# Kernel optimization log

Measured on AMD Instinct MI355X. Metric: run time of the kernel, lower is better.

Reference implementation:

```python
import jax, jax.numpy as jnp
import numpy as np

B, C, K = 8192, 4096, 4096
BK, BN = 1, 16          # block-sparse tile sizes (bk x bn)
KEEP = 0.3


def setup_inputs() -> dict:
    key = jax.random.key(0)
    kx, kw, kb, km = jax.random.split(key, 4)
    stdv = 1.0 / np.sqrt(C * K)  # reset_parameters uses 1/sqrt(C*K)
    x = jax.random.normal(kx, (B, C), dtype=jnp.float32)
    weight = jax.random.uniform(kw, (K, C), dtype=jnp.float32, minval=-stdv, maxval=stdv)
    # block mask on (K/bk, C/bn) grid, expanded to full weight shape
    blk = (jax.random.uniform(km, (K // BK, C // BN)) < KEEP).astype(jnp.float32)
    mask = jnp.repeat(jnp.repeat(blk, BK, axis=0), BN, axis=1)  # [K, C]
    weight = weight * mask
    bias = jax.random.uniform(kb, (K,), dtype=jnp.float32, minval=-stdv, maxval=stdv)
    return {"x": x, "weight": weight, "bias": bias}


def reference(x, weight, bias):
    # SparseLinearRelu forward (sparse-kernel path, attr='relu'):
    # y = relu(x @ W^T + b); zero blocks of W contribute nothing (skipped by kernel).
    return jax.nn.relu(jnp.dot(x, weight.T) + bias)
```

## Files before the change

kernel.cpp:

```cpp
#include <hip/hip_runtime.h>
#include <hip/hip_bf16.h>

typedef __attribute__((ext_vector_type(4))) float f32x4;
typedef __attribute__((ext_vector_type(8))) short bf16x8;
typedef __attribute__((ext_vector_type(4))) short bf16x4v;

#define M_DIM 8192
#define N_DIM 4096
#define K_DIM 4096
#define NX (M_DIM * K_DIM)
#define NW (N_DIM * K_DIM)

#define BM 256
#define BN 256
#define BK 64
#define NKT (K_DIM / BK)
#define THREADS 512

#define GLOAD_LDS16(g, l)                                                        \
  __builtin_amdgcn_global_load_lds(                                              \
      (const __attribute__((address_space(1))) void*)(g),                        \
      (__attribute__((address_space(3))) void*)(l), 16, 0, 0)

__global__ __launch_bounds__(256) void convert_bf16(const float* __restrict__ x,
                                                    const float* __restrict__ w,
                                                    short* __restrict__ ws) {
  const long stride = (long)gridDim.x * blockDim.x;
  const long total8 = ((long)NX + NW) / 8;
  for (long i = blockIdx.x * (long)blockDim.x + threadIdx.x; i < total8; i += stride) {
    const long base = i * 8;
    const float* src = (base < NX) ? (x + base) : (w + (base - NX));
    short* dst = ws + base;
    f32x4 a = *(const f32x4*)src;
    f32x4 b = *(const f32x4*)(src + 4);
    bf16x8 o;
    o[0] = (short)__bfloat16_as_ushort(__float2bfloat16(a[0]));
    o[1] = (short)__bfloat16_as_ushort(__float2bfloat16(a[1]));
    o[2] = (short)__bfloat16_as_ushort(__float2bfloat16(a[2]));
    o[3] = (short)__bfloat16_as_ushort(__float2bfloat16(a[3]));
    o[4] = (short)__bfloat16_as_ushort(__float2bfloat16(b[0]));
    o[5] = (short)__bfloat16_as_ushort(__float2bfloat16(b[1]));
    o[6] = (short)__bfloat16_as_ushort(__float2bfloat16(b[2]));
    o[7] = (short)__bfloat16_as_ushort(__float2bfloat16(b[3]));
    *(bf16x8*)dst = o;
  }
}

__global__ __launch_bounds__(THREADS, 2) void gemm256_bf16(
    const short* __restrict__ Abf,
    const short* __restrict__ Bbf,
    const float* __restrict__ bias,
    float* __restrict__ Y) {
  __shared__ short lds[2 * 32768];
  char* const ldsb = (char*)lds;

  const int tid  = threadIdx.x;
  const int lane = tid & 63;
  const int wave = tid >> 6;
  const int wm   = wave >> 2;
  const int wn   = wave & 3;

  const int lin = blockIdx.x + blockIdx.y * (N_DIM / BN);
  const int xcd = lin & 7;
  const int idx = lin >> 3;
  const int by = (xcd >> 1) * 8 + (idx >> 3);
  const int bx = (xcd & 1) * 8 + (idx & 7);
  const long rowA0 = (long)by * BM;
  const long rowB0 = (long)bx * BN;

  const int sg_col = (((lane & 7) ^ ((lane >> 3) & 7)) << 3);
  const int s_row  = wave * 8 + (lane >> 3);
  const int voff = s_row * K_DIM + sg_col;

  const short* uA = Abf + rowA0 * (long)K_DIM;
  const short* uB = Bbf + rowB0 * (long)K_DIM;

  const int offk0 = (lane & 15) * 128 + ((((lane >> 4)) ^ (lane & 7)) << 4);
  const int offk1 = (lane & 15) * 128 + (((4 + (lane >> 4)) ^ (lane & 7)) << 4);

#define STAGE_HALF(BOFF_, HALF_, TT) do {                                        \
    const short* u_ = ((HALF_) < 2 ? uA : uB) +                                  \
                      (long)(((HALF_) & 1) * 128) * K_DIM + (long)(TT) * BK;     \
    char* l_ = ldsb + (BOFF_) + ((HALF_) < 2 ? 0 : 32768) +                      \
               ((HALF_) & 1) * 16384 + wave * 1024;                              \
    GLOAD_LDS16(u_ + voff, l_);                                                  \
    GLOAD_LDS16(u_ + 64 * K_DIM + voff, l_ + 8192);                              \
  } while (0)

#define PH_READ_A(DST, BOFF_, MADD) do {                                         \
    const char* pa_ = ldsb + (BOFF_) + wm * 16384 + (MADD);                      \
    _Pragma("unroll")                                                            \
    for (int m_ = 0; m_ < 4; ++m_) {                                             \
      DST[m_][0] = *(const bf16x8*)(pa_ + m_ * 2048 + offk0);                    \
      DST[m_][1] = *(const bf16x8*)(pa_ + m_ * 2048 + offk1);                    \
    }                                                                            \
  } while (0)

#define PH_READ_B(DST, BOFF_, NADD) do {                                         \
    const char* pb_ = ldsb + (BOFF_) + 32768 + wn * 8192 + (NADD);               \
    _Pragma("unroll")                                                            \
    for (int n_ = 0; n_ < 2; ++n_) {                                             \
      DST[n_][0] = *(const bf16x8*)(pb_ + n_ * 2048 + offk0);                    \
      DST[n_][1] = *(const bf16x8*)(pb_ + n_ * 2048 + offk1);                    \
    }                                                                            \
  } while (0)

#define MFMA16(AF, BF, MB, NB) do {                                              \
    __builtin_amdgcn_s_setprio(1);                                               \
    _Pragma("unroll")                                                            \
    for (int kk_ = 0; kk_ < 2; ++kk_)                                            \
      _Pragma("unroll")                                                          \
      for (int m_ = 0; m_ < 4; ++m_)                                             \
        _Pragma("unroll")                                                        \
        for (int n_ = 0; n_ < 2; ++n_)                                           \
          acc[(MB) + m_][(NB) + n_] = __builtin_amdgcn_mfma_f32_16x16x32_bf16(   \
              AF[m_][kk_], BF[n_][kk_], acc[(MB) + m_][(NB) + n_], 0, 0, 0);     \
    __builtin_amdgcn_s_setprio(0);                                               \
  } while (0)

#define TILE(BOFF_, T, DO_ST, VM) do {                                           \
                               \
    PH_READ_A(af, BOFF_, 0);                                                     \
    PH_READ_B(bfr01, BOFF_, 0);                                                  \
    MFMA16(af, bfr01, 0, 0);                                                     \
    __builtin_amdgcn_s_barrier();                                                \
                                        \
    PH_READ_B(bfr23, BOFF_, 4096);                                               \
    MFMA16(af, bfr23, 0, 2);                                                     \
    __builtin_amdgcn_s_barrier();                                                \
                          \
    PH_READ_A(af, BOFF_, 8192);                                                  \
    if (DO_ST) { STAGE_HALF(BOFF_, 2, (T) + 2); STAGE_HALF(BOFF_, 3, (T) + 2); } \
    MFMA16(af, bfr01, 4, 0);                                                     \
    __builtin_amdgcn_s_barrier();                                                \
                   \
    if (DO_ST) { STAGE_HALF(BOFF_, 0, (T) + 2); STAGE_HALF(BOFF_, 1, (T) + 2); } \
    MFMA16(af, bfr23, 4, 2);                                                     \
    if ((VM) == 8)      asm volatile("s_waitcnt vmcnt(8)" ::: "memory");         \
    else if ((VM) == 0) asm volatile("s_waitcnt vmcnt(0)" ::: "memory");         \
    if ((VM) >= 0) __builtin_amdgcn_s_barrier();                                 \
  } while (0)

  f32x4 acc[8][4];
#pragma unroll
  for (int i = 0; i < 8; ++i)
#pragma unroll
    for (int j = 0; j < 4; ++j) acc[i][j] = (f32x4)0.0f;

  bf16x8 af[4][2], bfr01[2][2], bfr23[2][2];

  STAGE_HALF(0, 0, 0);
  STAGE_HALF(0, 1, 0);
  STAGE_HALF(0, 2, 0);
  STAGE_HALF(0, 3, 0);
  STAGE_HALF(65536, 2, 1);
  STAGE_HALF(65536, 3, 1);
  STAGE_HALF(65536, 0, 1);
  STAGE_HALF(65536, 1, 1);
  asm volatile("s_waitcnt vmcnt(8)" ::: "memory");
  __builtin_amdgcn_s_barrier();

  for (int tp = 0; tp < NKT / 2 - 1; ++tp) {
    const int t0 = 2 * tp;
    TILE(0,     t0,     1, 8);
    TILE(65536, t0 + 1, 1, 8);
  }
  TILE(0,     NKT - 2, 0, 0);
  TILE(65536, NKT - 1, 0, -1);

#undef TILE
#undef MFMA16
#undef PH_READ_B
#undef PH_READ_A
#undef STAGE_HALF

  {
    char* scr = ldsb + wave * 8192;
    const int c0 = lane & 15;
    const int r0 = (lane >> 4) * 4;
    const int rd_row = lane >> 3;
    const int rd_ch  = (lane & 7) * 16;
#pragma unroll
    for (int jp = 0; jp < 2; ++jp) {
      const long gcb = rowB0 + wn * 64 + jp * 32 + (lane & 7) * 4;
      const f32x4 bv4 = *(const f32x4*)&bias[gcb];
#pragma unroll
      for (int i = 0; i < 8; ++i) {
#pragma unroll
        for (int r = 0; r < 4; ++r) {
          *(float*)(scr + (r0 + r) * 144 + c0 * 4)      = acc[i][2 * jp + 0][r];
          *(float*)(scr + (r0 + r) * 144 + 64 + c0 * 4) = acc[i][2 * jp + 1][r];
        }
        f32x4 v0 = *(const f32x4*)(scr + rd_row * 144 + rd_ch);
        f32x4 v1 = *(const f32x4*)(scr + (8 + rd_row) * 144 + rd_ch);
        v0 += bv4;
        v1 += bv4;
#pragma unroll
        for (int e = 0; e < 4; ++e) {
          v0[e] = fmaxf(v0[e], 0.0f);
          v1[e] = fmaxf(v1[e], 0.0f);
        }
        const long gr = rowA0 + wm * 128 + i * 16;
        *(f32x4*)&Y[(gr + rd_row) * (long)N_DIM + gcb]     = v0;
        *(f32x4*)&Y[(gr + 8 + rd_row) * (long)N_DIM + gcb] = v1;
      }
    }
  }
}

#define FBM 128
#define FBK 32
#define FLDSS 40
__global__ __launch_bounds__(256) void fallback_gemm(
    const float* __restrict__ X, const float* __restrict__ W,
    const float* __restrict__ bias, float* __restrict__ Y) {
  __shared__ short As[FBM * FLDSS];
  __shared__ short Bs[FBM * FLDSS];
  const int tid = threadIdx.x, lane = tid & 63, wave = tid >> 6;
  const int wm = (wave >> 1) * 64, wn = (wave & 1) * 64;
  const long rowA0 = (long)blockIdx.y * FBM, rowB0 = (long)blockIdx.x * FBM;
  const int srow = tid >> 3, scol = (tid & 7) * 4;
  const float* Aptr = X + (rowA0 + srow) * (long)K_DIM + scol;
  const float* Bptr = W + (rowB0 + srow) * (long)K_DIM + scol;
  f32x4 ra[4], rb[4];
#pragma unroll
  for (int i = 0; i < 4; ++i) {
    ra[i] = *(const f32x4*)(Aptr + (long)i * 32 * K_DIM);
    rb[i] = *(const f32x4*)(Bptr + (long)i * 32 * K_DIM);
  }
  f32x4 acc[4][4];
#pragma unroll
  for (int i = 0; i < 4; ++i)
#pragma unroll
    for (int j = 0; j < 4; ++j) acc[i][j] = (f32x4)0.0f;
  for (int kt = 0; kt < K_DIM / FBK; ++kt) {
    __syncthreads();
#pragma unroll
    for (int i = 0; i < 4; ++i) {
      bf16x4v pa, pb;
#pragma unroll
      for (int j = 0; j < 4; ++j) {
        pa[j] = (short)__bfloat16_as_ushort(__float2bfloat16(ra[i][j]));
        pb[j] = (short)__bfloat16_as_ushort(__float2bfloat16(rb[i][j]));
      }
      *(bf16x4v*)&As[(i * 32 + srow) * FLDSS + scol] = pa;
      *(bf16x4v*)&Bs[(i * 32 + srow) * FLDSS + scol] = pb;
    }
    if (kt + 1 < K_DIM / FBK) {
      const float* An = Aptr + (kt + 1) * FBK;
      const float* Bn = Bptr + (kt + 1) * FBK;
#pragma unroll
      for (int i = 0; i < 4; ++i) {
        ra[i] = *(const f32x4*)(An + (long)i * 32 * K_DIM);
        rb[i] = *(const f32x4*)(Bn + (long)i * 32 * K_DIM);
      }
    }
    __syncthreads();
    bf16x8 af[4], bfr[4];
#pragma unroll
    for (int i = 0; i < 4; ++i) {
      af[i]  = *(const bf16x8*)&As[(wm + i * 16 + (lane & 15)) * FLDSS + (lane >> 4) * 8];
      bfr[i] = *(const bf16x8*)&Bs[(wn + i * 16 + (lane & 15)) * FLDSS + (lane >> 4) * 8];
    }
#pragma unroll
    for (int i = 0; i < 4; ++i)
#pragma unroll
      for (int j = 0; j < 4; ++j)
        acc[i][j] = __builtin_amdgcn_mfma_f32_16x16x32_bf16(af[i], bfr[j], acc[i][j], 0, 0, 0);
  }
  const int r0 = (lane >> 4) * 4, c0 = lane & 15;
#pragma unroll
  for (int j = 0; j < 4; ++j) {
    const long gc = rowB0 + wn + j * 16 + c0;
    const float bv = bias[gc];
#pragma unroll
    for (int i = 0; i < 4; ++i) {
      const long gr0 = rowA0 + wm + i * 16 + r0;
#pragma unroll
      for (int r = 0; r < 4; ++r) {
        float v = acc[i][j][r] + bv;
        Y[(gr0 + r) * (long)N_DIM + gc] = fmaxf(v, 0.0f);
      }
    }
  }
}

extern "C" void kernel_launch(void* const* d_in, const int* in_sizes, int n_in,
                              void* d_out, int out_size, void* d_ws, size_t ws_size,
                              hipStream_t stream) {
  const float* x = (const float*)d_in[0];
  const float* w = (const float*)d_in[1];
  const float* b = (const float*)d_in[2];
  float* y = (float*)d_out;

  const size_t need = (size_t)(NX + NW) * sizeof(short);
  if (ws_size >= need) {
    short* ws = (short*)d_ws;
    convert_bf16<<<2048, 256, 0, stream>>>(x, w, ws);
    dim3 grid(N_DIM / BN, M_DIM / BM);
    gemm256_bf16<<<grid, dim3(THREADS), 0, stream>>>(ws, ws + NX, b, y);
  } else {
    dim3 grid(N_DIM / FBM, M_DIM / FBM);
    fallback_gemm<<<grid, dim3(256), 0, stream>>>(x, w, b, y);
  }
}
```

Before: 251.9 us.

## Shrink GEMM tile to 256x128x32 with four waves and triple-buffered LDS

```diff
diff --git a/kernel.cpp b/kernel.cpp
--- a/kernel.cpp
+++ b/kernel.cpp
@@ -12,10 +12,11 @@
 #define NW (N_DIM * K_DIM)
 
 #define BM 256
-#define BN 256
-#define BK 64
+#define BN 128
+#define BK 32
 #define NKT (K_DIM / BK)
-#define THREADS 512
+#define THREADS 256
+#define SLOT_SZ 24576
 
 #define GLOAD_LDS16(g, l)                                                        \
   __builtin_amdgcn_global_load_lds(                                              \
@@ -46,97 +47,68 @@
   }
 }
 
-__global__ __launch_bounds__(THREADS, 2) void gemm256_bf16(
+__global__ __launch_bounds__(THREADS, 2) void gemm2_bf16(
     const short* __restrict__ Abf,
     const short* __restrict__ Bbf,
     const float* __restrict__ bias,
     float* __restrict__ Y) {
-  __shared__ short lds[2 * 32768];
+  __shared__ short lds[3 * SLOT_SZ / 2];
   char* const ldsb = (char*)lds;
 
   const int tid  = threadIdx.x;
   const int lane = tid & 63;
   const int wave = tid >> 6;
-  const int wm   = wave >> 2;
-  const int wn   = wave & 3;
+  const int wm   = wave >> 1;
+  const int wn   = wave & 1;
 
   const int lin = blockIdx.x + blockIdx.y * (N_DIM / BN);
   const int xcd = lin & 7;
   const int idx = lin >> 3;
-  const int by = (xcd >> 1) * 8 + (idx >> 3);
-  const int bx = (xcd & 1) * 8 + (idx & 7);
+  const int by = (xcd & 3) * 8 + (idx >> 4);
+  const int bx = (xcd >> 2) * 16 + (idx & 15);
   const long rowA0 = (long)by * BM;
   const long rowB0 = (long)bx * BN;
 
-  const int sg_col = (((lane & 7) ^ ((lane >> 3) & 7)) << 3);
-  const int s_row  = wave * 8 + (lane >> 3);
-  const int voff = s_row * K_DIM + sg_col;
+  const int h_st  = (tid & 7) ^ ((tid >> 3) & 7);
+  const int voff  = (2 * (tid >> 3) + (h_st >> 2)) * K_DIM + (h_st & 3) * 8;
 
   const short* uA = Abf + rowA0 * (long)K_DIM;
   const short* uB = Bbf + rowB0 * (long)K_DIM;
 
-  const int offk0 = (lane & 15) * 128 + ((((lane >> 4)) ^ (lane & 7)) << 4);
-  const int offk1 = (lane & 15) * 128 + (((4 + (lane >> 4)) ^ (lane & 7)) << 4);
-
-#define STAGE_HALF(BOFF_, HALF_, TT) do {                                        \
-    const short* u_ = ((HALF_) < 2 ? uA : uB) +                                  \
-                      (long)(((HALF_) & 1) * 128) * K_DIM + (long)(TT) * BK;     \
-    char* l_ = ldsb + (BOFF_) + ((HALF_) < 2 ? 0 : 32768) +                      \
-               ((HALF_) & 1) * 16384 + wave * 1024;                              \
-    GLOAD_LDS16(u_ + voff, l_);                                                  \
-    GLOAD_LDS16(u_ + 64 * K_DIM + voff, l_ + 8192);                              \
+  const int physoff = ((lane & 15) >> 1) * 128 +
+                      ((((((lane & 1) << 2) | (lane >> 4))) ^ ((lane >> 1) & 7)) << 4);
+
+#define STAGE2(SLOT_, TT) do {                                                   \
+    const short* ga_ = uA + (long)(TT) * BK + voff;                              \
+    char* la_ = ldsb + (SLOT_) * SLOT_SZ + wave * 1024;                          \
+    GLOAD_LDS16(ga_, la_);                                                       \
+    GLOAD_LDS16(ga_ + 64 * (long)K_DIM, la_ + 4096);                             \
+    GLOAD_LDS16(ga_ + 128 * (long)K_DIM, la_ + 8192);                            \
+    GLOAD_LDS16(ga_ + 192 * (long)K_DIM, la_ + 12288);                           \
+    const short* gb_ = uB + (long)(TT) * BK + voff;                              \
+    char* lb_ = ldsb + (SLOT_) * SLOT_SZ + 16384 + wave * 1024;                  \
+    GLOAD_LDS16(gb_, lb_);                                                       \
+    GLOAD_LDS16(gb_ + 64 * (long)K_DIM, lb_ + 4096);                             \
   } while (0)
 
-#define PH_READ_A(DST, BOFF_, MADD) do {                                         \
-    const char* pa_ = ldsb + (BOFF_) + wm * 16384 + (MADD);                      \
+#define TILE2(SLOT_, STSLOT_, T, DO_ST, VM) do {                                 \
+    const char* base_ = ldsb + (SLOT_) * SLOT_SZ;                                \
     _Pragma("unroll")                                                            \
-    for (int m_ = 0; m_ < 4; ++m_) {                                             \
-      DST[m_][0] = *(const bf16x8*)(pa_ + m_ * 2048 + offk0);                    \
-      DST[m_][1] = *(const bf16x8*)(pa_ + m_ * 2048 + offk1);                    \
-    }                                                                            \
-  } while (0)
-
-#define PH_READ_B(DST, BOFF_, NADD) do {                                         \
-    const char* pb_ = ldsb + (BOFF_) + 32768 + wn * 8192 + (NADD);               \
+    for (int mf_ = 0; mf_ < 8; ++mf_)                                            \
+      af[mf_] = *(const bf16x8*)(base_ + wm * 8192 + mf_ * 1024 + physoff);      \
     _Pragma("unroll")                                                            \
-    for (int n_ = 0; n_ < 2; ++n_) {                                             \
-      DST[n_][0] = *(const bf16x8*)(pb_ + n_ * 2048 + offk0);                    \
-      DST[n_][1] = *(const bf16x8*)(pb_ + n_ * 2048 + offk1);                    \
-    }                                                                            \
-  } while (0)
-
-#define MFMA16(AF, BF, MB, NB) do {                                              \
+    for (int nf_ = 0; nf_ < 4; ++nf_)                                            \
+      bf[nf_] = *(const bf16x8*)(base_ + 16384 + wn * 4096 + nf_ * 1024 + physoff);\
+    if (DO_ST) STAGE2(STSLOT_, (T) + 2);                                         \
     __builtin_amdgcn_s_setprio(1);                                               \
     _Pragma("unroll")                                                            \
-    for (int kk_ = 0; kk_ < 2; ++kk_)                                            \
+    for (int mf_ = 0; mf_ < 8; ++mf_)                                            \
       _Pragma("unroll")                                                          \
-      for (int m_ = 0; m_ < 4; ++m_)                                             \
-        _Pragma("unroll")                                                        \
-        for (int n_ = 0; n_ < 2; ++n_)                                           \
-          acc[(MB) + m_][(NB) + n_] = __builtin_amdgcn_mfma_f32_16x16x32_bf16(   \
-              AF[m_][kk_], BF[n_][kk_], acc[(MB) + m_][(NB) + n_], 0, 0, 0);     \
+      for (int nf_ = 0; nf_ < 4; ++nf_)                                          \
+        acc[mf_][nf_] = __builtin_amdgcn_mfma_f32_16x16x32_bf16(                 \
+            af[mf_], bf[nf_], acc[mf_][nf_], 0, 0, 0);                           \
     __builtin_amdgcn_s_setprio(0);                                               \
-  } while (0)
-
-#define TILE(BOFF_, T, DO_ST, VM) do {                                           \
-                               \
-    PH_READ_A(af, BOFF_, 0);                                                     \
-    PH_READ_B(bfr01, BOFF_, 0);                                                  \
-    MFMA16(af, bfr01, 0, 0);                                                     \
-    __builtin_amdgcn_s_barrier();                                                \
-                                        \
-    PH_READ_B(bfr23, BOFF_, 4096);                                               \
-    MFMA16(af, bfr23, 0, 2);                                                     \
-    __builtin_amdgcn_s_barrier();                                                \
-                          \
-    PH_READ_A(af, BOFF_, 8192);                                                  \
-    if (DO_ST) { STAGE_HALF(BOFF_, 2, (T) + 2); STAGE_HALF(BOFF_, 3, (T) + 2); } \
-    MFMA16(af, bfr01, 4, 0);                                                     \
-    __builtin_amdgcn_s_barrier();                                                \
-                   \
-    if (DO_ST) { STAGE_HALF(BOFF_, 0, (T) + 2); STAGE_HALF(BOFF_, 1, (T) + 2); } \
-    MFMA16(af, bfr23, 4, 2);                                                     \
-    if ((VM) == 8)      asm volatile("s_waitcnt vmcnt(8)" ::: "memory");         \
+    if ((VM) == 6)      asm volatile("s_waitcnt vmcnt(6)" ::: "memory");         \
     else if ((VM) == 0) asm volatile("s_waitcnt vmcnt(0)" ::: "memory");         \
     if ((VM) >= 0) __builtin_amdgcn_s_barrier();                                 \
   } while (0)
@@ -147,32 +119,25 @@
 #pragma unroll
     for (int j = 0; j < 4; ++j) acc[i][j] = (f32x4)0.0f;
 
-  bf16x8 af[4][2], bfr01[2][2], bfr23[2][2];
-
-  STAGE_HALF(0, 0, 0);
-  STAGE_HALF(0, 1, 0);
-  STAGE_HALF(0, 2, 0);
-  STAGE_HALF(0, 3, 0);
-  STAGE_HALF(65536, 2, 1);
-  STAGE_HALF(65536, 3, 1);
-  STAGE_HALF(65536, 0, 1);
-  STAGE_HALF(65536, 1, 1);
-  asm volatile("s_waitcnt vmcnt(8)" ::: "memory");
+  bf16x8 af[8], bf[4];
+
+  STAGE2(0, 0);
+  STAGE2(1, 1);
+  asm volatile("s_waitcnt vmcnt(6)" ::: "memory");
   __builtin_amdgcn_s_barrier();
 
-  for (int tp = 0; tp < NKT / 2 - 1; ++tp) {
-    const int t0 = 2 * tp;
-    TILE(0,     t0,     1, 8);
-    TILE(65536, t0 + 1, 1, 8);
-  }
-  TILE(0,     NKT - 2, 0, 0);
-  TILE(65536, NKT - 1, 0, -1);
-
-#undef TILE
-#undef MFMA16
-#undef PH_READ_B
-#undef PH_READ_A
-#undef STAGE_HALF
+  for (int tt = 0; tt < NKT / 3; ++tt) {
+    const int t0 = 3 * tt;
+    TILE2(0, 2, t0,     1, 6);
+    TILE2(1, 0, t0 + 1, 1, 6);
+    TILE2(2, 1, t0 + 2, 1, 6);
+  }
+  TILE2(0, 0, NKT - 2, 0, 0);
+  TILE2(1, 0, NKT - 1, 0, -1);
+  __builtin_amdgcn_s_barrier();
+
+#undef TILE2
+#undef STAGE2
 
   {
     char* scr = ldsb + wave * 8192;
@@ -298,7 +263,7 @@
     short* ws = (short*)d_ws;
     convert_bf16<<<2048, 256, 0, stream>>>(x, w, ws);
     dim3 grid(N_DIM / BN, M_DIM / BM);
-    gemm256_bf16<<<grid, dim3(THREADS), 0, stream>>>(ws, ws + NX, b, y);
+    gemm2_bf16<<<grid, dim3(THREADS), 0, stream>>>(ws, ws + NX, b, y);
   } else {
     dim3 grid(N_DIM / FBM, M_DIM / FBM);
     fallback_gemm<<<grid, dim3(256), 0, stream>>>(x, w, b, y);
```

New measurement: 291.9 us. 15.9% more time.
